# Kernel optimization log

Measured on AMD Instinct MI355X. Metric: run time of the kernel, lower is better.

## Reference

```python
import math
import jax, jax.numpy as jnp
import numpy as np

N_HEADS = 16

def setup_inputs() -> dict:
    key = jax.random.key(0)
    qkv = jax.random.normal(key, (4, 3072, 2048), dtype=jnp.float32)
    return {"qkv": qkv}

def reference(qkv):
    bs, width, length = qkv.shape
    ch = width // (3 * N_HEADS)
    # [bs*H, 3*ch, L] -> split into q, k, v of [bs*H, ch, L]
    qkv_r = qkv.reshape(bs * N_HEADS, 3 * ch, length)
    q, k, v = qkv_r[:, :ch], qkv_r[:, ch:2 * ch], qkv_r[:, 2 * ch:]
    scale = 1.0 / math.sqrt(math.sqrt(ch))
    # scores: [bs*H, T, S]
    weight = jnp.einsum('bct,bcs->bts', q * scale, k * scale)
    weight = jax.nn.softmax(weight, axis=-1)
    a = jnp.einsum('bts,bcs->bct', weight, v)
    return a.reshape(bs, -1, length)
```

## Files before the change

### kernel.cpp

```cpp
#include <hip/hip_runtime.h>
#include <cstdint>

typedef _Float16 half8 __attribute__((ext_vector_type(8)));
typedef __fp16 fp16x2 __attribute__((ext_vector_type(2)));
typedef float f32x4 __attribute__((ext_vector_type(4)));

#define HSTRIDE 131072
#define KOFF    ((size_t)64 * HSTRIDE)
#define VOFF    ((size_t)128 * HSTRIDE)

__device__ __forceinline__ float fast_exp2(float x) {
    return __builtin_amdgcn_exp2f(x);
}

__device__ __forceinline__ uint32_t pkrtz(float a, float b) {
    fp16x2 h = __builtin_amdgcn_cvt_pkrtz(a, b);
    return __builtin_bit_cast(uint32_t, h);
}

__global__ __launch_bounds__(256) void prep_kernel(const float* __restrict__ qkv,
                                                   _Float16* __restrict__ ws)
{
    __shared__ float Lf[64 * 67];

    const int tid  = threadIdx.x;
    const int lane = tid & 63;
    const int wave = tid >> 6;
    const int bid  = blockIdx.x;

    if (bid < 2048) {
        const int head  = (bid >> 5) & 63;
        const int chunk = bid & 31;
        const int b4 = head >> 4, h = head & 15;
        const float* src = qkv + (((size_t)(b4 * 3072 + h * 192 + 64)) << 11)
                         + chunk * 64;

#pragma unroll
        for (int k = 0; k < 4; ++k) {
            int idx = k * 256 + tid;
            int c = idx >> 4;
            int t4 = (idx & 15) << 2;
            float4 f = *(const float4*)&src[(((size_t)c) << 11) + t4];
            float* d = &Lf[c * 67 + t4];
            d[0] = f.x; d[1] = f.y; d[2] = f.z; d[3] = f.w;
        }
        __syncthreads();

        const int q = lane >> 4, l15 = lane & 15;
        const int scol = wave * 16 + l15;
#pragma unroll
        for (int k = 0; k < 2; ++k) {
            uint32_t d[4];
#pragma unroll
            for (int j = 0; j < 4; ++j) {
                float a = Lf[(32 * k + 8 * q + 2 * j) * 67 + scol];
                float b = Lf[(32 * k + 8 * q + 2 * j + 1) * 67 + scol];
                d[j] = pkrtz(a, b);
            }
            size_t off = KOFF + (size_t)head * HSTRIDE
                       + (size_t)((((chunk * 4 + wave) * 2 + k) * 512) + lane * 8);
            *(uint4*)&ws[off] = make_uint4(d[0], d[1], d[2], d[3]);
        }
    } else {
        const int vb = bid - 2048;
        const int head = vb >> 5, chunk = vb & 31;
        const int b4 = head >> 4, h = head & 15;
        const float* src = qkv + (((size_t)(b4 * 3072 + h * 192 + 128)) << 11) + chunk * 64;
        const int q = lane >> 4, cl = lane & 15;
        const int c = wave * 16 + cl;
#pragma unroll
        for (int k = 0; k < 2; ++k) {
            const float* p = &src[((size_t)c << 11) + k * 32 + q * 4];
            float4 f0 = *(const float4*)&p[0];
            float4 f1 = *(const float4*)&p[16];
            size_t off = VOFF + (size_t)head * HSTRIDE
                       + (size_t)(((chunk * 2 + k) * 4 + wave) * 512 + lane * 8);
            *(uint4*)&ws[off] = make_uint4(pkrtz(f0.x, f0.y), pkrtz(f0.z, f0.w),
                                           pkrtz(f1.x, f1.y), pkrtz(f1.z, f1.w));
        }
    }
}

__launch_bounds__(256, 2)
__global__ void attn_kernel(const float* __restrict__ qkv,
                            const _Float16* __restrict__ ws, float* __restrict__ out)
{
    const int tid  = threadIdx.x;
    const int lane = tid & 63;
    const int wave = tid >> 6;
    const int l15  = lane & 15;
    const int quad = lane >> 4;

    const int bid  = blockIdx.x;
    const int head = bid & 63;
    const int tblk = bid >> 6;
    const int T0   = tblk * 256;
    const int b4   = head >> 4;
    const int h    = head & 15;

    const _Float16* Kt = ws + KOFF + (size_t)head * HSTRIDE + lane * 8;
    const _Float16* Vt = ws + VOFF + (size_t)head * HSTRIDE + lane * 8;
    const float*    Qg = qkv + ((size_t)(b4 * 3072 + h * 192) << 11);
    const float kQ = 0.125f * 1.44269504088896340736f;

    f32x4 Oacc[4][4];
#pragma unroll
    for (int ct = 0; ct < 4; ++ct)
#pragma unroll
        for (int nt = 0; nt < 4; ++nt) Oacc[ct][nt] = (f32x4)0.f;
    f32x4 Lacc[4];
#pragma unroll
    for (int nt = 0; nt < 4; ++nt) Lacc[nt] = (f32x4)0.f;
    const f32x4 fz = (f32x4)0.f;

    half8 ones;
#pragma unroll
    for (int j = 0; j < 8; ++j) ones[j] = (_Float16)1.0f;

    half8 kfA[2][2], kfB[2][2], vfA[4], vfB[4];

#pragma unroll
    for (int st = 0; st < 2; ++st)
#pragma unroll
        for (int ks = 0; ks < 2; ++ks) {
            kfA[st][ks] = *(const half8*)(Kt + (size_t)(0 * 4 + st * 2 + ks) * 512);
            kfB[st][ks] = *(const half8*)(Kt + (size_t)(1 * 4 + st * 2 + ks) * 512);
        }
#pragma unroll
    for (int ct = 0; ct < 4; ++ct) {
        vfA[ct] = *(const half8*)(Vt + (size_t)(0 * 4 + ct) * 512);
        vfB[ct] = *(const half8*)(Vt + (size_t)(1 * 4 + ct) * 512);
    }

    half8 qb[4][2];
#pragma unroll
    for (int nt = 0; nt < 4; ++nt) {
        const int t = T0 + wave * 64 + nt * 16 + l15;
#pragma unroll
        for (int ks = 0; ks < 2; ++ks) {
            float f[8];
#pragma unroll
            for (int j = 0; j < 8; ++j)
                f[j] = Qg[((size_t)(ks * 32 + quad * 8 + j) << 11) + t];
            uint4 u = make_uint4(pkrtz(f[0] * kQ, f[1] * kQ), pkrtz(f[2] * kQ, f[3] * kQ),
                                 pkrtz(f[4] * kQ, f[5] * kQ), pkrtz(f[6] * kQ, f[7] * kQ));
            qb[nt][ks] = __builtin_bit_cast(half8, u);
        }
    }

    half8 pf[4];

    {
        f32x4 Sa[4], Sb[4];
#pragma unroll
        for (int nt = 0; nt < 4; ++nt) {
            f32x4 t0 = __builtin_amdgcn_mfma_f32_16x16x32_f16(kfA[0][0], qb[nt][0], fz, 0, 0, 0);
            Sa[nt]   = __builtin_amdgcn_mfma_f32_16x16x32_f16(kfA[0][1], qb[nt][1], t0, 0, 0, 0);
            f32x4 t1 = __builtin_amdgcn_mfma_f32_16x16x32_f16(kfA[1][0], qb[nt][0], fz, 0, 0, 0);
            Sb[nt]   = __builtin_amdgcn_mfma_f32_16x16x32_f16(kfA[1][1], qb[nt][1], t1, 0, 0, 0);
        }
#pragma unroll
        for (int nt = 0; nt < 4; ++nt) {
            uint4 u = make_uint4(pkrtz(fast_exp2(Sa[nt][0]), fast_exp2(Sa[nt][1])),
                                 pkrtz(fast_exp2(Sa[nt][2]), fast_exp2(Sa[nt][3])),
                                 pkrtz(fast_exp2(Sb[nt][0]), fast_exp2(Sb[nt][1])),
                                 pkrtz(fast_exp2(Sb[nt][2]), fast_exp2(Sb[nt][3])));
            pf[nt] = __builtin_bit_cast(half8, u);
        }
    }

    auto body = [&](int i, half8 (&kfC)[2][2], half8 (&kfN)[2][2],
                    half8 (&vfN)[4], bool pre) {
        if (pre) {
#pragma unroll
            for (int st = 0; st < 2; ++st)
#pragma unroll
                for (int ks = 0; ks < 2; ++ks)
                    kfN[st][ks] = *(const half8*)(Kt + (size_t)((i + 1) * 4 + st * 2 + ks) * 512);
        }
#pragma unroll
        for (int ct = 0; ct < 4; ++ct)
#pragma unroll
            for (int nt = 0; nt < 4; ++nt)
                Oacc[ct][nt] = __builtin_amdgcn_mfma_f32_16x16x32_f16(
                    vfN[ct], pf[nt], Oacc[ct][nt], 0, 0, 0);
#pragma unroll
        for (int nt = 0; nt < 4; ++nt)
            Lacc[nt] = __builtin_amdgcn_mfma_f32_16x16x32_f16(ones, pf[nt], Lacc[nt], 0, 0, 0);
        if (pre) {
#pragma unroll
            for (int ct = 0; ct < 4; ++ct)
                vfN[ct] = *(const half8*)(Vt + (size_t)((i + 1) * 4 + ct) * 512);
        }
        f32x4 Sa[4], Sb[4];
#pragma unroll
        for (int nt = 0; nt < 4; ++nt) {
            f32x4 t0 = __builtin_amdgcn_mfma_f32_16x16x32_f16(kfC[0][0], qb[nt][0], fz, 0, 0, 0);
            Sa[nt]   = __builtin_amdgcn_mfma_f32_16x16x32_f16(kfC[0][1], qb[nt][1], t0, 0, 0, 0);
            f32x4 t1 = __builtin_amdgcn_mfma_f32_16x16x32_f16(kfC[1][0], qb[nt][0], fz, 0, 0, 0);
            Sb[nt]   = __builtin_amdgcn_mfma_f32_16x16x32_f16(kfC[1][1], qb[nt][1], t1, 0, 0, 0);
        }
#pragma unroll
        for (int nt = 0; nt < 4; ++nt) {
            uint4 u = make_uint4(pkrtz(fast_exp2(Sa[nt][0]), fast_exp2(Sa[nt][1])),
                                 pkrtz(fast_exp2(Sa[nt][2]), fast_exp2(Sa[nt][3])),
                                 pkrtz(fast_exp2(Sb[nt][0]), fast_exp2(Sb[nt][1])),
                                 pkrtz(fast_exp2(Sb[nt][2]), fast_exp2(Sb[nt][3])));
            pf[nt] = __builtin_bit_cast(half8, u);
        }
    };

    for (int m = 0; m < 31; ++m) {
        body(2 * m + 1, kfB, kfA, vfA, true);
        body(2 * m + 2, kfA, kfB, vfB, true);
    }
    body(63, kfB, kfA, vfA, false);

#pragma unroll
    for (int ct = 0; ct < 4; ++ct)
#pragma unroll
        for (int nt = 0; nt < 4; ++nt)
            Oacc[ct][nt] = __builtin_amdgcn_mfma_f32_16x16x32_f16(
                vfB[ct], pf[nt], Oacc[ct][nt], 0, 0, 0);
#pragma unroll
    for (int nt = 0; nt < 4; ++nt)
        Lacc[nt] = __builtin_amdgcn_mfma_f32_16x16x32_f16(ones, pf[nt], Lacc[nt], 0, 0, 0);

    float inv[4];
#pragma unroll
    for (int nt = 0; nt < 4; ++nt) inv[nt] = 1.f / Lacc[nt][0];

    float* ob = out + (((size_t)(b4 * 1024 + h * 64)) << 11) + T0 + wave * 64;
#pragma unroll
    for (int ct = 0; ct < 4; ++ct)
#pragma unroll
        for (int nt = 0; nt < 4; ++nt) {
            f32x4 o = Oacc[ct][nt];
#pragma unroll
            for (int r = 0; r < 4; ++r)
                ob[((size_t)(ct * 16 + quad * 4 + r) << 11) + nt * 16 + l15] = o[r] * inv[nt];
        }
}

extern "C" void kernel_launch(void* const* d_in, const int* in_sizes, int n_in,
                              void* d_out, int out_size, void* d_ws, size_t ws_size,
                              hipStream_t stream) {
    const float* qkv = (const float*)d_in[0];
    float* out = (float*)d_out;
    _Float16* ws = (_Float16*)d_ws;
    prep_kernel<<<dim3(4096), dim3(256), 0, stream>>>(qkv, ws);
    attn_kernel<<<dim3(512), dim3(256), 0, stream>>>(qkv, ws, out);
}
```

Measured before the change: 215.9 us.

## Software-pipeline exp2 with QK and PV MFMAs and interleave via sched_group_barrier

```diff
diff --git a/kernel.cpp b/kernel.cpp
--- a/kernel.cpp
+++ b/kernel.cpp
@@ -117,20 +117,18 @@
 #pragma unroll
     for (int j = 0; j < 8; ++j) ones[j] = (_Float16)1.0f;
 
-    half8 kfA[2][2], kfB[2][2], vfA[4], vfB[4];
+    half8 kf0[2][2], kf1[2][2], vf0[4], vf1[4];
 
 #pragma unroll
     for (int st = 0; st < 2; ++st)
 #pragma unroll
         for (int ks = 0; ks < 2; ++ks) {
-            kfA[st][ks] = *(const half8*)(Kt + (size_t)(0 * 4 + st * 2 + ks) * 512);
-            kfB[st][ks] = *(const half8*)(Kt + (size_t)(1 * 4 + st * 2 + ks) * 512);
-        }
-#pragma unroll
-    for (int ct = 0; ct < 4; ++ct) {
-        vfA[ct] = *(const half8*)(Vt + (size_t)(0 * 4 + ct) * 512);
-        vfB[ct] = *(const half8*)(Vt + (size_t)(1 * 4 + ct) * 512);
-    }
+            kf0[st][ks] = *(const half8*)(Kt + (size_t)(0 * 4 + st * 2 + ks) * 512);
+            kf1[st][ks] = *(const half8*)(Kt + (size_t)(1 * 4 + st * 2 + ks) * 512);
+        }
+#pragma unroll
+    for (int ct = 0; ct < 4; ++ct)
+        vf0[ct] = *(const half8*)(Vt + (size_t)(0 * 4 + ct) * 512);
 
     half8 qb[4][2];
 #pragma unroll
@@ -148,83 +146,84 @@
         }
     }
 
-    half8 pf[4];
-
-    {
-        f32x4 Sa[4], Sb[4];
+    f32x4 SaS[4], SbS[4];
+#pragma unroll
+    for (int nt = 0; nt < 4; ++nt) {
+        f32x4 t0 = __builtin_amdgcn_mfma_f32_16x16x32_f16(kf0[0][0], qb[nt][0], fz, 0, 0, 0);
+        SaS[nt]  = __builtin_amdgcn_mfma_f32_16x16x32_f16(kf0[0][1], qb[nt][1], t0, 0, 0, 0);
+        f32x4 t1 = __builtin_amdgcn_mfma_f32_16x16x32_f16(kf0[1][0], qb[nt][0], fz, 0, 0, 0);
+        SbS[nt]  = __builtin_amdgcn_mfma_f32_16x16x32_f16(kf0[1][1], qb[nt][1], t1, 0, 0, 0);
+    }
+
+    auto body = [&](int i, half8 (&kfC)[2][2], half8 (&kfN)[2][2],
+                    half8 (&vfC)[4], half8 (&vfN)[4], bool preK) {
+        if (preK) {
+#pragma unroll
+            for (int st = 0; st < 2; ++st)
+#pragma unroll
+                for (int ks = 0; ks < 2; ++ks)
+                    kfN[st][ks] = *(const half8*)(Kt + (size_t)((i + 2) * 4 + st * 2 + ks) * 512);
+        }
+#pragma unroll
+        for (int ct = 0; ct < 4; ++ct)
+            vfN[ct] = *(const half8*)(Vt + (size_t)((i + 1) * 4 + ct) * 512);
+
 #pragma unroll
         for (int nt = 0; nt < 4; ++nt) {
-            f32x4 t0 = __builtin_amdgcn_mfma_f32_16x16x32_f16(kfA[0][0], qb[nt][0], fz, 0, 0, 0);
-            Sa[nt]   = __builtin_amdgcn_mfma_f32_16x16x32_f16(kfA[0][1], qb[nt][1], t0, 0, 0, 0);
-            f32x4 t1 = __builtin_amdgcn_mfma_f32_16x16x32_f16(kfA[1][0], qb[nt][0], fz, 0, 0, 0);
-            Sb[nt]   = __builtin_amdgcn_mfma_f32_16x16x32_f16(kfA[1][1], qb[nt][1], t1, 0, 0, 0);
-        }
-#pragma unroll
-        for (int nt = 0; nt < 4; ++nt) {
-            uint4 u = make_uint4(pkrtz(fast_exp2(Sa[nt][0]), fast_exp2(Sa[nt][1])),
-                                 pkrtz(fast_exp2(Sa[nt][2]), fast_exp2(Sa[nt][3])),
-                                 pkrtz(fast_exp2(Sb[nt][0]), fast_exp2(Sb[nt][1])),
-                                 pkrtz(fast_exp2(Sb[nt][2]), fast_exp2(Sb[nt][3])));
-            pf[nt] = __builtin_bit_cast(half8, u);
-        }
-    }
-
-    auto body = [&](int i, half8 (&kfC)[2][2], half8 (&kfN)[2][2],
-                    half8 (&vfN)[4], bool pre) {
-        if (pre) {
-#pragma unroll
-            for (int st = 0; st < 2; ++st)
-#pragma unroll
-                for (int ks = 0; ks < 2; ++ks)
-                    kfN[st][ks] = *(const half8*)(Kt + (size_t)((i + 1) * 4 + st * 2 + ks) * 512);
-        }
+            float e0 = fast_exp2(SaS[nt][0]);
+            float e1 = fast_exp2(SaS[nt][1]);
+            float e2 = fast_exp2(SaS[nt][2]);
+            float e3 = fast_exp2(SaS[nt][3]);
+            float e4 = fast_exp2(SbS[nt][0]);
+            float e5 = fast_exp2(SbS[nt][1]);
+            float e6 = fast_exp2(SbS[nt][2]);
+            float e7 = fast_exp2(SbS[nt][3]);
+            uint4 u = make_uint4(pkrtz(e0, e1), pkrtz(e2, e3),
+                                 pkrtz(e4, e5), pkrtz(e6, e7));
+            half8 pf = __builtin_bit_cast(half8, u);
+#pragma unroll
+            for (int ct = 0; ct < 4; ++ct)
+                Oacc[ct][nt] = __builtin_amdgcn_mfma_f32_16x16x32_f16(
+                    vfC[ct], pf, Oacc[ct][nt], 0, 0, 0);
+            Lacc[nt] = __builtin_amdgcn_mfma_f32_16x16x32_f16(ones, pf, Lacc[nt], 0, 0, 0);
+            f32x4 t0 = __builtin_amdgcn_mfma_f32_16x16x32_f16(kfC[0][0], qb[nt][0], fz, 0, 0, 0);
+            SaS[nt]  = __builtin_amdgcn_mfma_f32_16x16x32_f16(kfC[0][1], qb[nt][1], t0, 0, 0, 0);
+            f32x4 t1 = __builtin_amdgcn_mfma_f32_16x16x32_f16(kfC[1][0], qb[nt][0], fz, 0, 0, 0);
+            SbS[nt]  = __builtin_amdgcn_mfma_f32_16x16x32_f16(kfC[1][1], qb[nt][1], t1, 0, 0, 0);
+        }
+
+#pragma unroll
+        for (int g = 0; g < 12; ++g) {
+            __builtin_amdgcn_sched_group_barrier(0x008, 3, 0);
+            __builtin_amdgcn_sched_group_barrier(0x402, 4, 0);
+        }
+    };
+
+    for (int m = 0; m < 31; ++m) {
+        body(2 * m,     kf1, kf0, vf0, vf1, true);
+        body(2 * m + 1, kf0, kf1, vf1, vf0, true);
+    }
+    body(62, kf1, kf0, vf0, vf1, false);
+
+#pragma unroll
+    for (int nt = 0; nt < 4; ++nt) {
+        float e0 = fast_exp2(SaS[nt][0]);
+        float e1 = fast_exp2(SaS[nt][1]);
+        float e2 = fast_exp2(SaS[nt][2]);
+        float e3 = fast_exp2(SaS[nt][3]);
+        float e4 = fast_exp2(SbS[nt][0]);
+        float e5 = fast_exp2(SbS[nt][1]);
+        float e6 = fast_exp2(SbS[nt][2]);
+        float e7 = fast_exp2(SbS[nt][3]);
+        uint4 u = make_uint4(pkrtz(e0, e1), pkrtz(e2, e3),
+                             pkrtz(e4, e5), pkrtz(e6, e7));
+        half8 pf = __builtin_bit_cast(half8, u);
 #pragma unroll
         for (int ct = 0; ct < 4; ++ct)
-#pragma unroll
-            for (int nt = 0; nt < 4; ++nt)
-                Oacc[ct][nt] = __builtin_amdgcn_mfma_f32_16x16x32_f16(
-                    vfN[ct], pf[nt], Oacc[ct][nt], 0, 0, 0);
-#pragma unroll
-        for (int nt = 0; nt < 4; ++nt)
-            Lacc[nt] = __builtin_amdgcn_mfma_f32_16x16x32_f16(ones, pf[nt], Lacc[nt], 0, 0, 0);
-        if (pre) {
-#pragma unroll
-            for (int ct = 0; ct < 4; ++ct)
-                vfN[ct] = *(const half8*)(Vt + (size_t)((i + 1) * 4 + ct) * 512);
-        }
-        f32x4 Sa[4], Sb[4];
-#pragma unroll
-        for (int nt = 0; nt < 4; ++nt) {
-            f32x4 t0 = __builtin_amdgcn_mfma_f32_16x16x32_f16(kfC[0][0], qb[nt][0], fz, 0, 0, 0);
-            Sa[nt]   = __builtin_amdgcn_mfma_f32_16x16x32_f16(kfC[0][1], qb[nt][1], t0, 0, 0, 0);
-            f32x4 t1 = __builtin_amdgcn_mfma_f32_16x16x32_f16(kfC[1][0], qb[nt][0], fz, 0, 0, 0);
-            Sb[nt]   = __builtin_amdgcn_mfma_f32_16x16x32_f16(kfC[1][1], qb[nt][1], t1, 0, 0, 0);
-        }
-#pragma unroll
-        for (int nt = 0; nt < 4; ++nt) {
-            uint4 u = make_uint4(pkrtz(fast_exp2(Sa[nt][0]), fast_exp2(Sa[nt][1])),
-                                 pkrtz(fast_exp2(Sa[nt][2]), fast_exp2(Sa[nt][3])),
-                                 pkrtz(fast_exp2(Sb[nt][0]), fast_exp2(Sb[nt][1])),
-                                 pkrtz(fast_exp2(Sb[nt][2]), fast_exp2(Sb[nt][3])));
-            pf[nt] = __builtin_bit_cast(half8, u);
-        }
-    };
-
-    for (int m = 0; m < 31; ++m) {
-        body(2 * m + 1, kfB, kfA, vfA, true);
-        body(2 * m + 2, kfA, kfB, vfB, true);
-    }
-    body(63, kfB, kfA, vfA, false);
-
-#pragma unroll
-    for (int ct = 0; ct < 4; ++ct)
-#pragma unroll
-        for (int nt = 0; nt < 4; ++nt)
             Oacc[ct][nt] = __builtin_amdgcn_mfma_f32_16x16x32_f16(
-                vfB[ct], pf[nt], Oacc[ct][nt], 0, 0, 0);
-#pragma unroll
-    for (int nt = 0; nt < 4; ++nt)
-        Lacc[nt] = __builtin_amdgcn_mfma_f32_16x16x32_f16(ones, pf[nt], Lacc[nt], 0, 0, 0);
+                vf1[ct], pf, Oacc[ct][nt], 0, 0, 0);
+        Lacc[nt] = __builtin_amdgcn_mfma_f32_16x16x32_f16(ones, pf, Lacc[nt], 0, 0, 0);
+    }
 
     float inv[4];
 #pragma unroll
```

After: 221.8 us. 1.03x slower.

## Halve query tile per block, double grid, compute row sums with VALU

Applied to the files above, without the earlier changes.

```diff
diff --git a/kernel.cpp b/kernel.cpp
--- a/kernel.cpp
+++ b/kernel.cpp
@@ -81,7 +81,7 @@
     }
 }
 
-__launch_bounds__(256, 2)
+__launch_bounds__(256, 4)
 __global__ void attn_kernel(const float* __restrict__ qkv,
                             const _Float16* __restrict__ ws, float* __restrict__ out)
 {
@@ -94,7 +94,7 @@
     const int bid  = blockIdx.x;
     const int head = bid & 63;
     const int tblk = bid >> 6;
-    const int T0   = tblk * 256;
+    const int T0   = tblk * 128;
     const int b4   = head >> 4;
     const int h    = head & 15;
 
@@ -103,19 +103,13 @@
     const float*    Qg = qkv + ((size_t)(b4 * 3072 + h * 192) << 11);
     const float kQ = 0.125f * 1.44269504088896340736f;
 
-    f32x4 Oacc[4][4];
+    f32x4 Oacc[4][2];
 #pragma unroll
     for (int ct = 0; ct < 4; ++ct)
 #pragma unroll
-        for (int nt = 0; nt < 4; ++nt) Oacc[ct][nt] = (f32x4)0.f;
-    f32x4 Lacc[4];
-#pragma unroll
-    for (int nt = 0; nt < 4; ++nt) Lacc[nt] = (f32x4)0.f;
+        for (int nt = 0; nt < 2; ++nt) Oacc[ct][nt] = (f32x4)0.f;
+    float lacc[2] = {0.f, 0.f};
     const f32x4 fz = (f32x4)0.f;
-
-    half8 ones;
-#pragma unroll
-    for (int j = 0; j < 8; ++j) ones[j] = (_Float16)1.0f;
 
     half8 kfA[2][2], kfB[2][2], vfA[4], vfB[4];
 
@@ -132,10 +126,10 @@
         vfB[ct] = *(const half8*)(Vt + (size_t)(1 * 4 + ct) * 512);
     }
 
-    half8 qb[4][2];
-#pragma unroll
-    for (int nt = 0; nt < 4; ++nt) {
-        const int t = T0 + wave * 64 + nt * 16 + l15;
+    half8 qb[2][2];
+#pragma unroll
+    for (int nt = 0; nt < 2; ++nt) {
+        const int t = T0 + wave * 32 + nt * 16 + l15;
 #pragma unroll
         for (int ks = 0; ks < 2; ++ks) {
             float f[8];
@@ -148,23 +142,30 @@
         }
     }
 
-    half8 pf[4];
+    half8 pf[2];
 
     {
-        f32x4 Sa[4], Sb[4];
-#pragma unroll
-        for (int nt = 0; nt < 4; ++nt) {
+        f32x4 Sa[2], Sb[2];
+#pragma unroll
+        for (int nt = 0; nt < 2; ++nt) {
             f32x4 t0 = __builtin_amdgcn_mfma_f32_16x16x32_f16(kfA[0][0], qb[nt][0], fz, 0, 0, 0);
             Sa[nt]   = __builtin_amdgcn_mfma_f32_16x16x32_f16(kfA[0][1], qb[nt][1], t0, 0, 0, 0);
             f32x4 t1 = __builtin_amdgcn_mfma_f32_16x16x32_f16(kfA[1][0], qb[nt][0], fz, 0, 0, 0);
             Sb[nt]   = __builtin_amdgcn_mfma_f32_16x16x32_f16(kfA[1][1], qb[nt][1], t1, 0, 0, 0);
         }
 #pragma unroll
-        for (int nt = 0; nt < 4; ++nt) {
-            uint4 u = make_uint4(pkrtz(fast_exp2(Sa[nt][0]), fast_exp2(Sa[nt][1])),
-                                 pkrtz(fast_exp2(Sa[nt][2]), fast_exp2(Sa[nt][3])),
-                                 pkrtz(fast_exp2(Sb[nt][0]), fast_exp2(Sb[nt][1])),
-                                 pkrtz(fast_exp2(Sb[nt][2]), fast_exp2(Sb[nt][3])));
+        for (int nt = 0; nt < 2; ++nt) {
+            float e0 = fast_exp2(Sa[nt][0]);
+            float e1 = fast_exp2(Sa[nt][1]);
+            float e2 = fast_exp2(Sa[nt][2]);
+            float e3 = fast_exp2(Sa[nt][3]);
+            float e4 = fast_exp2(Sb[nt][0]);
+            float e5 = fast_exp2(Sb[nt][1]);
+            float e6 = fast_exp2(Sb[nt][2]);
+            float e7 = fast_exp2(Sb[nt][3]);
+            lacc[nt] += ((e0 + e1) + (e2 + e3)) + ((e4 + e5) + (e6 + e7));
+            uint4 u = make_uint4(pkrtz(e0, e1), pkrtz(e2, e3),
+                                 pkrtz(e4, e5), pkrtz(e6, e7));
             pf[nt] = __builtin_bit_cast(half8, u);
         }
     }
@@ -181,31 +182,35 @@
 #pragma unroll
         for (int ct = 0; ct < 4; ++ct)
 #pragma unroll
-            for (int nt = 0; nt < 4; ++nt)
+            for (int nt = 0; nt < 2; ++nt)
                 Oacc[ct][nt] = __builtin_amdgcn_mfma_f32_16x16x32_f16(
                     vfN[ct], pf[nt], Oacc[ct][nt], 0, 0, 0);
-#pragma unroll
-        for (int nt = 0; nt < 4; ++nt)
-            Lacc[nt] = __builtin_amdgcn_mfma_f32_16x16x32_f16(ones, pf[nt], Lacc[nt], 0, 0, 0);
         if (pre) {
 #pragma unroll
             for (int ct = 0; ct < 4; ++ct)
                 vfN[ct] = *(const half8*)(Vt + (size_t)((i + 1) * 4 + ct) * 512);
         }
-        f32x4 Sa[4], Sb[4];
-#pragma unroll
-        for (int nt = 0; nt < 4; ++nt) {
+        f32x4 Sa[2], Sb[2];
+#pragma unroll
+        for (int nt = 0; nt < 2; ++nt) {
             f32x4 t0 = __builtin_amdgcn_mfma_f32_16x16x32_f16(kfC[0][0], qb[nt][0], fz, 0, 0, 0);
             Sa[nt]   = __builtin_amdgcn_mfma_f32_16x16x32_f16(kfC[0][1], qb[nt][1], t0, 0, 0, 0);
             f32x4 t1 = __builtin_amdgcn_mfma_f32_16x16x32_f16(kfC[1][0], qb[nt][0], fz, 0, 0, 0);
             Sb[nt]   = __builtin_amdgcn_mfma_f32_16x16x32_f16(kfC[1][1], qb[nt][1], t1, 0, 0, 0);
         }
 #pragma unroll
-        for (int nt = 0; nt < 4; ++nt) {
-            uint4 u = make_uint4(pkrtz(fast_exp2(Sa[nt][0]), fast_exp2(Sa[nt][1])),
-                                 pkrtz(fast_exp2(Sa[nt][2]), fast_exp2(Sa[nt][3])),
-                                 pkrtz(fast_exp2(Sb[nt][0]), fast_exp2(Sb[nt][1])),
-                                 pkrtz(fast_exp2(Sb[nt][2]), fast_exp2(Sb[nt][3])));
+        for (int nt = 0; nt < 2; ++nt) {
+            float e0 = fast_exp2(Sa[nt][0]);
+            float e1 = fast_exp2(Sa[nt][1]);
+            float e2 = fast_exp2(Sa[nt][2]);
+            float e3 = fast_exp2(Sa[nt][3]);
+            float e4 = fast_exp2(Sb[nt][0]);
+            float e5 = fast_exp2(Sb[nt][1]);
+            float e6 = fast_exp2(Sb[nt][2]);
+            float e7 = fast_exp2(Sb[nt][3]);
+            lacc[nt] += ((e0 + e1) + (e2 + e3)) + ((e4 + e5) + (e6 + e7));
+            uint4 u = make_uint4(pkrtz(e0, e1), pkrtz(e2, e3),
+                                 pkrtz(e4, e5), pkrtz(e6, e7));
             pf[nt] = __builtin_bit_cast(half8, u);
         }
     };
@@ -219,22 +224,24 @@
 #pragma unroll
     for (int ct = 0; ct < 4; ++ct)
 #pragma unroll
-        for (int nt = 0; nt < 4; ++nt)
+        for (int nt = 0; nt < 2; ++nt)
             Oacc[ct][nt] = __builtin_amdgcn_mfma_f32_16x16x32_f16(
                 vfB[ct], pf[nt], Oacc[ct][nt], 0, 0, 0);
-#pragma unroll
-    for (int nt = 0; nt < 4; ++nt)
-        Lacc[nt] = __builtin_amdgcn_mfma_f32_16x16x32_f16(ones, pf[nt], Lacc[nt], 0, 0, 0);
-
-    float inv[4];
-#pragma unroll
-    for (int nt = 0; nt < 4; ++nt) inv[nt] = 1.f / Lacc[nt][0];
-
-    float* ob = out + (((size_t)(b4 * 1024 + h * 64)) << 11) + T0 + wave * 64;
+
+    float inv[2];
+#pragma unroll
+    for (int nt = 0; nt < 2; ++nt) {
+        float v = lacc[nt];
+        v += __shfl_xor(v, 16, 64);
+        v += __shfl_xor(v, 32, 64);
+        inv[nt] = 1.f / v;
+    }
+
+    float* ob = out + (((size_t)(b4 * 1024 + h * 64)) << 11) + T0 + wave * 32;
 #pragma unroll
     for (int ct = 0; ct < 4; ++ct)
 #pragma unroll
-        for (int nt = 0; nt < 4; ++nt) {
+        for (int nt = 0; nt < 2; ++nt) {
             f32x4 o = Oacc[ct][nt];
 #pragma unroll
             for (int r = 0; r < 4; ++r)
@@ -249,5 +256,5 @@
     float* out = (float*)d_out;
     _Float16* ws = (_Float16*)d_ws;
     prep_kernel<<<dim3(4096), dim3(256), 0, stream>>>(qkv, ws);
-    attn_kernel<<<dim3(512), dim3(256), 0, stream>>>(qkv, ws, out);
-}
+    attn_kernel<<<dim3(1024), dim3(256), 0, stream>>>(qkv, ws, out);
+}
```

After: 231.5 us. 7.2% more time.
